# Kernel tuning notes

Hardware: AMD Instinct MI355X
Metric: run time of the kernel (lower is better)

Reference implementation:

```python
import jax, jax.numpy as jnp
import numpy as np

N_NODES = 100000
N_EDGES = 1600000
NFEAT, NHID, NOUT = 128, 64, 32


def setup_inputs() -> dict:
    key = jax.random.key(0)
    ks = jax.random.split(key, 8)
    x = jax.random.normal(ks[0], (N_NODES, NFEAT), dtype=jnp.float32)
    adj_vals = jax.random.uniform(ks[1], (N_EDGES,), dtype=jnp.float32)
    W1 = jax.random.normal(ks[2], (NFEAT, NHID), dtype=jnp.float32) * (1.0 / np.sqrt(NFEAT))
    b1 = jnp.zeros((NHID,), dtype=jnp.float32)
    W2 = jax.random.normal(ks[3], (NHID, NOUT), dtype=jnp.float32) * (1.0 / np.sqrt(NHID))
    b2 = jnp.zeros((NOUT,), dtype=jnp.float32)
    edge_src = jax.random.randint(ks[4], (N_EDGES,), 0, N_NODES, dtype=jnp.int32)
    edge_dst = jax.random.randint(ks[5], (N_EDGES,), 0, N_NODES, dtype=jnp.int32)
    return {"x": x, "adj_vals": adj_vals, "W1": W1, "b1": b1, "W2": W2,
            "b2": b2, "edge_src": edge_src, "edge_dst": edge_dst}


def spmm(vals, src, dst, dense, n_nodes):
    # out[i, :] = sum_{e : dst[e]==i} vals[e] * dense[src[e], :]
    gathered = dense[src] * vals[:, None]          # [E, D] gather (memory-bound)
    return jax.ops.segment_sum(gathered, dst, num_segments=n_nodes)


def reference(x, adj_vals, W1, b1, W2, b2, edge_src, edge_dst):
    # GraphConvolution 1: support = x @ W1; out = adj @ support + b1; relu
    h = spmm(adj_vals, edge_src, edge_dst, x @ W1, N_NODES) + b1
    h = jax.nn.relu(h)
    # dropout is identity in eval mode (training=False)
    # GraphConvolution 2
    out = spmm(adj_vals, edge_src, edge_dst, h @ W2, N_NODES) + b2
    return out
```

## Files before the change

### kernel.cpp

```cpp
#include <hip/hip_runtime.h>
#include <hip/hip_fp16.h>

#define N_NODES 100000
#define N_EDGES 1600000
#define NFEAT 128
#define NHID 64
#define NOUT 32

#define NPB 256
#define NB ((N_NODES + NPB - 1) / NPB)
#define CAP 4608
#define CCH 4096
#define NCH ((N_EDGES + CCH - 1) / CCH)
#define G1B ((N_NODES / 16 + 7) / 8)

typedef _Float16 half8 __attribute__((ext_vector_type(8)));
typedef float floatx4 __attribute__((ext_vector_type(4)));

__device__ __forceinline__ int wave_incl_scan(int v, int lane) {
#pragma unroll
    for (int d = 1; d < 64; d <<= 1) {
        int t = __shfl_up(v, d, 64);
        if (lane >= d) v += t;
    }
    return v;
}
__device__ __forceinline__ int block_excl_scan_512(int tsum, int tid, int* w8) {
    const int lane = tid & 63, wid = tid >> 6;
    int incl = wave_incl_scan(tsum, lane);
    if (lane == 63) w8[wid] = incl;
    __syncthreads();
    int wbase = 0;
#pragma unroll
    for (int i = 0; i < 7; ++i)
        if (wid > i) wbase += w8[i];
    return wbase + incl - tsum;
}

__global__ __launch_bounds__(64) void prep_kernel(const float* __restrict__ W1,
                                                  const float* __restrict__ W2,
                                                  __half* __restrict__ wfrag,
                                                  __half* __restrict__ w2frag,
                                                  int* __restrict__ gcur) {
    const int l = threadIdx.x;
    const int b = blockIdx.x;
    if (b < 16) {
        const int ks = b >> 2, ct = b & 3;
        const int kb = ks * 32 + (l >> 4) * 8;
        const int c  = ct * 16 + (l & 15);
        union { __half2 h2[4]; uint4 u; } pk;
#pragma unroll
        for (int j = 0; j < 4; ++j)
            pk.h2[j] = __floats2half2_rn(W1[(kb + 2 * j) * NHID + c],
                                         W1[(kb + 2 * j + 1) * NHID + c]);
        *(uint4*)&wfrag[((size_t)b * 64 + l) * 8] = pk.u;
    } else if (b < 20) {
        const int bb = b - 16;
        const int ks = bb >> 1, ct = bb & 1;
        const int kb = ks * 32 + (l >> 4) * 8;
        const int c  = ct * 16 + (l & 15);
        union { __half2 h2[4]; uint4 u; } pk;
#pragma unroll
        for (int j = 0; j < 4; ++j)
            pk.h2[j] = __floats2half2_rn(W2[(kb + 2 * j) * NOUT + c],
                                         W2[(kb + 2 * j + 1) * NOUT + c]);
        *(uint4*)&w2frag[((size_t)bb * 64 + l) * 8] = pk.u;
    } else {
        int i = (b - 20) * 64 + l;
        if (i < NB) gcur[i] = i * CAP;
    }
}

__global__ __launch_bounds__(512) void g1cs_kernel(const float* __restrict__ x,
                                                   const __half* __restrict__ wfrag,
                                                   __half* __restrict__ support,
                                                   const float* __restrict__ vals,
                                                   const int* __restrict__ src,
                                                   const int* __restrict__ dst,
                                                   int* __restrict__ gcur,
                                                   uint2* __restrict__ recsC) {
    __shared__ int cnt[NB];
    __shared__ int pos[NB];
    const int tid = threadIdx.x;

    if (blockIdx.x < NCH) {
        const int cbase0 = blockIdx.x * CCH;
        for (int i = tid; i < NB; i += 512) cnt[i] = 0;
        int dstv[CCH / 512];
        __syncthreads();
#pragma unroll
        for (int k = 0; k < CCH / 512; ++k) {
            int e = cbase0 + k * 512 + tid;
            int d = (e < N_EDGES) ? dst[e] : -1;
            dstv[k] = d;
            if (d >= 0) atomicAdd(&cnt[d >> 8], 1);
        }
        __syncthreads();
        for (int b = tid; b < NB; b += 512) {
            int c = cnt[b];
            pos[b] = c ? atomicAdd(&gcur[b], c) : 0;
        }
        __syncthreads();
#pragma unroll
        for (int k = 0; k < CCH / 512; ++k) {
            int e = cbase0 + k * 512 + tid;
            int d = dstv[k];
            if (d >= 0) {
                int b = d >> 8;
                int slot = atomicAdd(&pos[b], 1);
                if (slot < (b + 1) * CAP)
                    recsC[slot] = make_uint2((unsigned)src[e] |
                                             ((unsigned)(d & (NPB - 1)) << 17),
                                             __float_as_uint(vals[e]));
            }
        }
    } else {
        const int lane = tid & 63;
        const int tile = (blockIdx.x - NCH) * 8 + (tid >> 6);
        const int n0 = tile * 16;
        if (n0 >= N_NODES) return;

        half8 a[4][4];
#pragma unroll
        for (int ks = 0; ks < 4; ++ks)
#pragma unroll
            for (int ct = 0; ct < 4; ++ct)
                a[ks][ct] = *(const half8*)&wfrag[((size_t)(ks * 4 + ct) * 64 + lane) * 8];

        floatx4 acc[4];
#pragma unroll
        for (int ct = 0; ct < 4; ++ct) acc[ct] = (floatx4){0.f, 0.f, 0.f, 0.f};

        const int node = n0 + (lane & 15);
        const float* xrow = x + (size_t)node * NFEAT + (lane >> 4) * 8;

#pragma unroll
        for (int ks = 0; ks < 4; ++ks) {
            float4 f0 = *(const float4*)(xrow + ks * 32);
            float4 f1 = *(const float4*)(xrow + ks * 32 + 4);
            union { __half2 h2[4]; half8 v; } bv;
            bv.h2[0] = __floats2half2_rn(f0.x, f0.y);
            bv.h2[1] = __floats2half2_rn(f0.z, f0.w);
            bv.h2[2] = __floats2half2_rn(f1.x, f1.y);
            bv.h2[3] = __floats2half2_rn(f1.z, f1.w);
#pragma unroll
            for (int ct = 0; ct < 4; ++ct)
                acc[ct] = __builtin_amdgcn_mfma_f32_16x16x32_f16(a[ks][ct], bv.v, acc[ct], 0, 0, 0);
        }

        __half* srow = support + (size_t)node * NHID + (lane >> 4) * 4;
#pragma unroll
        for (int ct = 0; ct < 4; ++ct) {
            union { __half2 h2[2]; uint2 u; } pk;
            pk.h2[0] = __floats2half2_rn(acc[ct][0], acc[ct][1]);
            pk.h2[1] = __floats2half2_rn(acc[ct][2], acc[ct][3]);
            *(uint2*)&srow[ct * 16] = pk.u;
        }
    }
}

__global__ __launch_bounds__(512) void fine_sort_kernel(const int* __restrict__ gcur,
                                                        const uint2* __restrict__ recsC,
                                                        uint2* __restrict__ recs2,
                                                        int* __restrict__ offs,
                                                        int* __restrict__ ends) {
    __shared__ int cnt[NPB];
    __shared__ int cur[NPB];
    __shared__ int w8[8];
    const int tid = threadIdx.x;
    const int b = blockIdx.x;
    const int s = b * CAP;
    const int e = min(gcur[b], s + CAP);
    if (tid < NPB) cnt[tid] = 0;
    __syncthreads();
    for (int i = s + tid; i < e; i += 512)
        atomicAdd(&cnt[(recsC[i].x >> 17) & (NPB - 1)], 1);
    __syncthreads();
    int v = (tid < NPB) ? cnt[tid] : 0;
    int excl = block_excl_scan_512(v, tid, w8);
    if (tid < NPB) {
        cur[tid] = excl;
        const int node = b * NPB + tid;
        if (node < N_NODES) {
            offs[node] = s + excl;
            ends[node] = s + excl + v;
        }
    }
    __syncthreads();
    for (int i = s + tid; i < e; i += 512) {
        uint2 r = recsC[i];
        int dl = (r.x >> 17) & (NPB - 1);
        int p = atomicAdd(&cur[dl], 1);
        recs2[s + p] = make_uint2(r.x & 0x1FFFF, r.y);
    }
}

__global__ __launch_bounds__(256) void spmm1_kernel(const int* __restrict__ offs,
                                                    const int* __restrict__ ends,
                                                    const uint2* __restrict__ recs,
                                                    const __half* __restrict__ dense,
                                                    const float* __restrict__ b1,
                                                    __half* __restrict__ h) {
    __shared__ float red[4][8][65];
    const int tid = threadIdx.x;
    const int lane = tid & 63;
    const int wid = tid >> 6;
    const int d = blockIdx.x * 4 + wid;
    if (d >= N_NODES) return;
    const int g = lane >> 3, q = lane & 7;
    __half2 hacc[4];
#pragma unroll
    for (int j = 0; j < 4; ++j) hacc[j] = __half2half2(__float2half(0.f));

    const int start = offs[d], end = ends[d];
    for (int e = start + g; e < end; e += 8) {
        uint2 r = recs[e];
        __half2 hv2 = __half2half2(__float2half(__uint_as_float(r.y)));
        union { uint4 u; __half2 h2[4]; } rw;
        rw.u = *(const uint4*)((const char*)dense + ((size_t)r.x << 7) + (q << 4));
#pragma unroll
        for (int j = 0; j < 4; ++j)
            hacc[j] = __hfma2(rw.h2[j], hv2, hacc[j]);
    }
#pragma unroll
    for (int j = 0; j < 4; ++j) {
        float2 f = __half22float2(hacc[j]);
        red[wid][g][q * 8 + 2 * j]     = f.x;
        red[wid][g][q * 8 + 2 * j + 1] = f.y;
    }
    __builtin_amdgcn_wave_barrier();
    float s = 0.f;
#pragma unroll
    for (int gg = 0; gg < 8; ++gg) s += red[wid][gg][lane];
    float hv = fmaxf(s + b1[lane], 0.f);
    h[(size_t)d * NHID + lane] = __float2half(hv);
}

__global__ __launch_bounds__(256) void gemm2_kernel(const __half* __restrict__ h,
                                                    const __half* __restrict__ w2frag,
                                                    __half* __restrict__ s2) {
    const int lane = threadIdx.x & 63;
    const int tile = blockIdx.x * 4 + (threadIdx.x >> 6);
    const int n0 = tile * 16;
    if (n0 >= N_NODES) return;

    half8 a[2][2];
#pragma unroll
    for (int ks = 0; ks < 2; ++ks)
#pragma unroll
        for (int ct = 0; ct < 2; ++ct)
            a[ks][ct] = *(const half8*)&w2frag[((size_t)(ks * 2 + ct) * 64 + lane) * 8];

    floatx4 acc[2];
#pragma unroll
    for (int ct = 0; ct < 2; ++ct) acc[ct] = (floatx4){0.f, 0.f, 0.f, 0.f};

    const int node = n0 + (lane & 15);
    const __half* hrow = h + (size_t)node * NHID + (lane >> 4) * 8;

#pragma unroll
    for (int ks = 0; ks < 2; ++ks) {
        half8 bv = *(const half8*)(hrow + ks * 32);
#pragma unroll
        for (int ct = 0; ct < 2; ++ct)
            acc[ct] = __builtin_amdgcn_mfma_f32_16x16x32_f16(a[ks][ct], bv, acc[ct], 0, 0, 0);
    }

    __half* srow = s2 + (size_t)node * NOUT + (lane >> 4) * 4;
#pragma unroll
    for (int ct = 0; ct < 2; ++ct) {
        union { __half2 h2[2]; uint2 u; } pk;
        pk.h2[0] = __floats2half2_rn(acc[ct][0], acc[ct][1]);
        pk.h2[1] = __floats2half2_rn(acc[ct][2], acc[ct][3]);
        *(uint2*)&srow[ct * 16] = pk.u;
    }
}

__global__ __launch_bounds__(256) void spmm2_kernel(const int* __restrict__ offs,
                                                    const int* __restrict__ ends,
                                                    const uint2* __restrict__ recs,
                                                    const __half* __restrict__ dense,
                                                    const float* __restrict__ b2,
                                                    float* __restrict__ out) {
    __shared__ float red[4][16][33];
    const int tid = threadIdx.x;
    const int lane = tid & 63;
    const int wid = tid >> 6;
    const int d = blockIdx.x * 4 + wid;
    if (d >= N_NODES) return;
    const int g = lane >> 2, q = lane & 3;
    __half2 hacc[4];
#pragma unroll
    for (int j = 0; j < 4; ++j) hacc[j] = __half2half2(__float2half(0.f));

    const int start = offs[d], end = ends[d];
    for (int e = start + g; e < end; e += 16) {
        uint2 r = recs[e];
        __half2 hv2 = __half2half2(__float2half(__uint_as_float(r.y)));
        union { uint4 u; __half2 h2[4]; } rw;
        rw.u = *(const uint4*)((const char*)dense + ((size_t)r.x << 6) + (q << 4));
#pragma unroll
        for (int j = 0; j < 4; ++j)
            hacc[j] = __hfma2(rw.h2[j], hv2, hacc[j]);
    }
#pragma unroll
    for (int j = 0; j < 4; ++j) {
        float2 f = __half22float2(hacc[j]);
        red[wid][g][q * 8 + 2 * j]     = f.x;
        red[wid][g][q * 8 + 2 * j + 1] = f.y;
    }
    __builtin_amdgcn_wave_barrier();
    const int f = lane & 31, hi = lane >> 5;
    float s = 0.f;
#pragma unroll
    for (int t = 0; t < 8; ++t) s += red[wid][hi * 8 + t][f];
    s += __shfl_xor(s, 32, 64);
    if (hi == 0) out[(size_t)d * NOUT + f] = s + b2[f];
}

extern "C" void kernel_launch(void* const* d_in, const int* in_sizes, int n_in,
                              void* d_out, int out_size, void* d_ws, size_t ws_size,
                              hipStream_t stream) {
    const float* x        = (const float*)d_in[0];
    const float* adj_vals = (const float*)d_in[1];
    const float* W1       = (const float*)d_in[2];
    const float* b1       = (const float*)d_in[3];
    const float* W2       = (const float*)d_in[4];
    const float* b2       = (const float*)d_in[5];
    const int*   esrc     = (const int*)d_in[6];
    const int*   edst     = (const int*)d_in[7];
    float*       out      = (float*)d_out;

    char* W = (char*)d_ws;
    __half* support = (__half*)W;
    __half* h       = (__half*)(W + 12800000);
    uint2*  recsC   = (uint2*)(W + 25600000);
    uint2*  recs2   = (uint2*)(W + 25600000 + (size_t)NB * CAP * 8);
    int*    IW      = (int*)(W + 25600000 + 2 * (size_t)NB * CAP * 8);
    int*    offs    = IW;
    int*    ends    = IW + 100032;
    int*    gcur    = IW + 200064;
    __half* wfrag   = (__half*)(IW + 200064 + 512);
    __half* w2frag  = wfrag + 8192;
    __half* s2      = support;

    prep_kernel<<<20 + (NB + 63) / 64, 64, 0, stream>>>(W1, W2, wfrag, w2frag, gcur);

    g1cs_kernel<<<NCH + G1B, 512, 0, stream>>>(x, wfrag, support,
                                               adj_vals, esrc, edst, gcur, recsC);

    fine_sort_kernel<<<NB, 512, 0, stream>>>(gcur, recsC, recs2, offs, ends);

    spmm1_kernel<<<(N_NODES + 3) / 4, 256, 0, stream>>>(offs, ends, recs2,
                                                        support, b1, h);

    gemm2_kernel<<<(N_NODES / 16 + 3) / 4, 256, 0, stream>>>(h, w2frag, s2);

    spmm2_kernel<<<(N_NODES + 3) / 4, 256, 0, stream>>>(offs, ends, recs2,
                                                        s2, b2, out);
}
```

Measured before the change: 134.3 us.

## Split SpMM kernels into feature-column slices with more edges per wave

Both SpMM kernels now split the feature dimension into 16-column slices handled by separate blocks (4 slices for layer 1, 2 for layer 2). Each wave walks 32 edges at once, with two lanes per edge each loading 16 bytes. Slices run in block order, so each pass gathers from a narrower column band of the dense matrix, which may improve cache locality and gives more edge-level parallelism per node. The cost is that the edge records and offsets are read once per slice, and each gathered row access brings in only 32 bytes instead of a full row.

Result: slower. 225.7 us (+68.0%).

```diff
diff --git a/kernel.cpp b/kernel.cpp
--- a/kernel.cpp
+++ b/kernel.cpp
@@ -13,6 +13,7 @@
 #define CCH 4096
 #define NCH ((N_EDGES + CCH - 1) / CCH)
 #define G1B ((N_NODES / 16 + 7) / 8)
+#define SQB (N_NODES / 4)
 
 typedef _Float16 half8 __attribute__((ext_vector_type(8)));
 typedef float floatx4 __attribute__((ext_vector_type(4)));
@@ -201,23 +202,25 @@
                                                     const __half* __restrict__ dense,
                                                     const float* __restrict__ b1,
                                                     __half* __restrict__ h) {
-    __shared__ float red[4][8][65];
+    __shared__ float red[4][32][17];
     const int tid = threadIdx.x;
     const int lane = tid & 63;
     const int wid = tid >> 6;
-    const int d = blockIdx.x * 4 + wid;
-    if (d >= N_NODES) return;
-    const int g = lane >> 3, q = lane & 7;
+    const int slice = blockIdx.x / SQB;
+    const int nq = blockIdx.x - slice * SQB;
+    const int d = nq * 4 + wid;
+    const int p = lane >> 1, sub = lane & 1;
     __half2 hacc[4];
 #pragma unroll
     for (int j = 0; j < 4; ++j) hacc[j] = __half2half2(__float2half(0.f));
 
     const int start = offs[d], end = ends[d];
-    for (int e = start + g; e < end; e += 8) {
+    const char* dbase = (const char*)dense + slice * 32 + sub * 16;
+    for (int e = start + p; e < end; e += 32) {
         uint2 r = recs[e];
         __half2 hv2 = __half2half2(__float2half(__uint_as_float(r.y)));
         union { uint4 u; __half2 h2[4]; } rw;
-        rw.u = *(const uint4*)((const char*)dense + ((size_t)r.x << 7) + (q << 4));
+        rw.u = *(const uint4*)(dbase + ((size_t)r.x << 7));
 #pragma unroll
         for (int j = 0; j < 4; ++j)
             hacc[j] = __hfma2(rw.h2[j], hv2, hacc[j]);
@@ -225,15 +228,21 @@
 #pragma unroll
     for (int j = 0; j < 4; ++j) {
         float2 f = __half22float2(hacc[j]);
-        red[wid][g][q * 8 + 2 * j]     = f.x;
-        red[wid][g][q * 8 + 2 * j + 1] = f.y;
+        red[wid][p][sub * 8 + 2 * j]     = f.x;
+        red[wid][p][sub * 8 + 2 * j + 1] = f.y;
     }
     __builtin_amdgcn_wave_barrier();
+    const int c = lane & 15, chunk = lane >> 4;
     float s = 0.f;
 #pragma unroll
-    for (int gg = 0; gg < 8; ++gg) s += red[wid][gg][lane];
-    float hv = fmaxf(s + b1[lane], 0.f);
-    h[(size_t)d * NHID + lane] = __float2half(hv);
+    for (int t = 0; t < 8; ++t) s += red[wid][chunk * 8 + t][c];
+    s += __shfl_xor(s, 16, 64);
+    s += __shfl_xor(s, 32, 64);
+    if (chunk == 0) {
+        const int col = slice * 16 + c;
+        float hv = fmaxf(s + b1[col], 0.f);
+        h[(size_t)d * NHID + col] = __float2half(hv);
+    }
 }
 
 __global__ __launch_bounds__(256) void gemm2_kernel(const __half* __restrict__ h,
@@ -282,23 +291,25 @@
                                                     const __half* __restrict__ dense,
                                                     const float* __restrict__ b2,
                                                     float* __restrict__ out) {
-    __shared__ float red[4][16][33];
+    __shared__ float red[4][32][17];
     const int tid = threadIdx.x;
     const int lane = tid & 63;
     const int wid = tid >> 6;
-    const int d = blockIdx.x * 4 + wid;
-    if (d >= N_NODES) return;
-    const int g = lane >> 2, q = lane & 3;
+    const int slice = blockIdx.x / SQB;
+    const int nq = blockIdx.x - slice * SQB;
+    const int d = nq * 4 + wid;
+    const int p = lane >> 1, sub = lane & 1;
     __half2 hacc[4];
 #pragma unroll
     for (int j = 0; j < 4; ++j) hacc[j] = __half2half2(__float2half(0.f));
 
     const int start = offs[d], end = ends[d];
-    for (int e = start + g; e < end; e += 16) {
+    const char* dbase = (const char*)dense + slice * 32 + sub * 16;
+    for (int e = start + p; e < end; e += 32) {
         uint2 r = recs[e];
         __half2 hv2 = __half2half2(__float2half(__uint_as_float(r.y)));
         union { uint4 u; __half2 h2[4]; } rw;
-        rw.u = *(const uint4*)((const char*)dense + ((size_t)r.x << 6) + (q << 4));
+        rw.u = *(const uint4*)(dbase + ((size_t)r.x << 6));
 #pragma unroll
         for (int j = 0; j < 4; ++j)
             hacc[j] = __hfma2(rw.h2[j], hv2, hacc[j]);
@@ -306,16 +317,20 @@
 #pragma unroll
     for (int j = 0; j < 4; ++j) {
         float2 f = __half22float2(hacc[j]);
-        red[wid][g][q * 8 + 2 * j]     = f.x;
-        red[wid][g][q * 8 + 2 * j + 1] = f.y;
+        red[wid][p][sub * 8 + 2 * j]     = f.x;
+        red[wid][p][sub * 8 + 2 * j + 1] = f.y;
     }
     __builtin_amdgcn_wave_barrier();
-    const int f = lane & 31, hi = lane >> 5;
+    const int c = lane & 15, chunk = lane >> 4;
     float s = 0.f;
 #pragma unroll
-    for (int t = 0; t < 8; ++t) s += red[wid][hi * 8 + t][f];
+    for (int t = 0; t < 8; ++t) s += red[wid][chunk * 8 + t][c];
+    s += __shfl_xor(s, 16, 64);
     s += __shfl_xor(s, 32, 64);
-    if (hi == 0) out[(size_t)d * NOUT + f] = s + b2[f];
+    if (chunk == 0) {
+        const int col = slice * 16 + c;
+        out[(size_t)d * NOUT + col] = s + b2[col];
+    }
 }
 
 extern "C" void kernel_launch(void* const* d_in, const int* in_sizes, int n_in,
@@ -351,11 +366,9 @@
 
     fine_sort_kernel<<<NB, 512, 0, stream>>>(gcur, recsC, recs2, offs, ends);
 
-    spmm1_kernel<<<(N_NODES + 3) / 4, 256, 0, stream>>>(offs, ends, recs2,
-                                                        support, b1, h);
+    spmm1_kernel<<<4 * SQB, 256, 0, stream>>>(offs, ends, recs2, support, b1, h);
 
     gemm2_kernel<<<(N_NODES / 16 + 3) / 4, 256, 0, stream>>>(h, w2frag, s2);
 
-    spmm2_kernel<<<(N_NODES + 3) / 4, 256, 0, stream>>>(offs, ends, recs2,
-                                                        s2, b2, out);
-}
+    spmm2_kernel<<<2 * SQB, 256, 0, stream>>>(offs, ends, recs2, s2, b2, out);
+}
```

## Split hidden features into column slices and pack edge records to 32 bits

Applied to the files above, without the earlier changes.

The support and hidden matrices are stored as two 32-column slices, each laid out contiguously per node, and spmm1 runs as two passes, one per slice, with 64-byte rows. Each pass's gathered working set is half as large, which should give better L2 hit rates for the random gathers. Edge records are packed into one 32-bit word holding a 17-bit source index and a 15-bit half value with the sign bit dropped, since the values are non-negative. This halves record traffic in both spmm kernels, at the cost of reading the edge list twice in spmm1.

Result: slower. 148.6 us (+10.6%).

```diff
diff --git a/kernel.cpp b/kernel.cpp
--- a/kernel.cpp
+++ b/kernel.cpp
@@ -13,6 +13,7 @@
 #define CCH 4096
 #define NCH ((N_EDGES + CCH - 1) / CCH)
 #define G1B ((N_NODES / 16 + 7) / 8)
+#define SQB (N_NODES / 4)
 
 typedef _Float16 half8 __attribute__((ext_vector_type(8)));
 typedef float floatx4 __attribute__((ext_vector_type(4)));
@@ -148,20 +149,21 @@
                 acc[ct] = __builtin_amdgcn_mfma_f32_16x16x32_f16(a[ks][ct], bv.v, acc[ct], 0, 0, 0);
         }
 
-        __half* srow = support + (size_t)node * NHID + (lane >> 4) * 4;
 #pragma unroll
         for (int ct = 0; ct < 4; ++ct) {
+            __half* srow = support + (size_t)(ct >> 1) * N_NODES * 32 +
+                           (size_t)node * 32 + (ct & 1) * 16 + (lane >> 4) * 4;
             union { __half2 h2[2]; uint2 u; } pk;
             pk.h2[0] = __floats2half2_rn(acc[ct][0], acc[ct][1]);
             pk.h2[1] = __floats2half2_rn(acc[ct][2], acc[ct][3]);
-            *(uint2*)&srow[ct * 16] = pk.u;
+            *(uint2*)srow = pk.u;
         }
     }
 }
 
 __global__ __launch_bounds__(512) void fine_sort_kernel(const int* __restrict__ gcur,
                                                         const uint2* __restrict__ recsC,
-                                                        uint2* __restrict__ recs2,
+                                                        unsigned* __restrict__ recs2,
                                                         int* __restrict__ offs,
                                                         int* __restrict__ ends) {
     __shared__ int cnt[NPB];
@@ -190,34 +192,37 @@
     for (int i = s + tid; i < e; i += 512) {
         uint2 r = recsC[i];
         int dl = (r.x >> 17) & (NPB - 1);
+        unsigned hb = (unsigned)__half_as_ushort(__float2half(__uint_as_float(r.y))) & 0x7FFFu;
         int p = atomicAdd(&cur[dl], 1);
-        recs2[s + p] = make_uint2(r.x & 0x1FFFF, r.y);
+        recs2[s + p] = (r.x & 0x1FFFFu) | (hb << 17);
     }
 }
 
 __global__ __launch_bounds__(256) void spmm1_kernel(const int* __restrict__ offs,
                                                     const int* __restrict__ ends,
-                                                    const uint2* __restrict__ recs,
-                                                    const __half* __restrict__ dense,
+                                                    const unsigned* __restrict__ recs,
+                                                    const __half* __restrict__ support,
                                                     const float* __restrict__ b1,
                                                     __half* __restrict__ h) {
-    __shared__ float red[4][8][65];
+    __shared__ float red[4][16][33];
     const int tid = threadIdx.x;
     const int lane = tid & 63;
     const int wid = tid >> 6;
-    const int d = blockIdx.x * 4 + wid;
-    if (d >= N_NODES) return;
-    const int g = lane >> 3, q = lane & 7;
+    const int slice = blockIdx.x / SQB;
+    const int nq = blockIdx.x - slice * SQB;
+    const int d = nq * 4 + wid;
+    const int g = lane >> 2, q4 = lane & 3;
     __half2 hacc[4];
 #pragma unroll
     for (int j = 0; j < 4; ++j) hacc[j] = __half2half2(__float2half(0.f));
 
     const int start = offs[d], end = ends[d];
-    for (int e = start + g; e < end; e += 8) {
-        uint2 r = recs[e];
-        __half2 hv2 = __half2half2(__float2half(__uint_as_float(r.y)));
+    const char* dbase = (const char*)(support + (size_t)slice * N_NODES * 32) + (q4 << 4);
+    for (int e = start + g; e < end; e += 16) {
+        unsigned r = recs[e];
+        __half2 hv2 = __half2half2(__ushort_as_half((unsigned short)(r >> 17)));
         union { uint4 u; __half2 h2[4]; } rw;
-        rw.u = *(const uint4*)((const char*)dense + ((size_t)r.x << 7) + (q << 4));
+        rw.u = *(const uint4*)(dbase + ((size_t)(r & 0x1FFFFu) << 6));
 #pragma unroll
         for (int j = 0; j < 4; ++j)
             hacc[j] = __hfma2(rw.h2[j], hv2, hacc[j]);
@@ -225,15 +230,19 @@
 #pragma unroll
     for (int j = 0; j < 4; ++j) {
         float2 f = __half22float2(hacc[j]);
-        red[wid][g][q * 8 + 2 * j]     = f.x;
-        red[wid][g][q * 8 + 2 * j + 1] = f.y;
+        red[wid][g][q4 * 8 + 2 * j]     = f.x;
+        red[wid][g][q4 * 8 + 2 * j + 1] = f.y;
     }
     __builtin_amdgcn_wave_barrier();
+    const int c = lane & 31, chunk = lane >> 5;
     float s = 0.f;
 #pragma unroll
-    for (int gg = 0; gg < 8; ++gg) s += red[wid][gg][lane];
-    float hv = fmaxf(s + b1[lane], 0.f);
-    h[(size_t)d * NHID + lane] = __float2half(hv);
+    for (int t = 0; t < 8; ++t) s += red[wid][chunk * 8 + t][c];
+    s += __shfl_xor(s, 32, 64);
+    if (chunk == 0) {
+        float hv = fmaxf(s + b1[slice * 32 + c], 0.f);
+        h[(size_t)slice * N_NODES * 32 + (size_t)d * 32 + c] = __float2half(hv);
+    }
 }
 
 __global__ __launch_bounds__(256) void gemm2_kernel(const __half* __restrict__ h,
@@ -256,11 +265,11 @@
     for (int ct = 0; ct < 2; ++ct) acc[ct] = (floatx4){0.f, 0.f, 0.f, 0.f};
 
     const int node = n0 + (lane & 15);
-    const __half* hrow = h + (size_t)node * NHID + (lane >> 4) * 8;
+    const __half* h0 = h + (size_t)node * 32 + (lane >> 4) * 8;
 
 #pragma unroll
     for (int ks = 0; ks < 2; ++ks) {
-        half8 bv = *(const half8*)(hrow + ks * 32);
+        half8 bv = *(const half8*)(h0 + (size_t)ks * N_NODES * 32);
 #pragma unroll
         for (int ct = 0; ct < 2; ++ct)
             acc[ct] = __builtin_amdgcn_mfma_f32_16x16x32_f16(a[ks][ct], bv, acc[ct], 0, 0, 0);
@@ -278,7 +287,7 @@
 
 __global__ __launch_bounds__(256) void spmm2_kernel(const int* __restrict__ offs,
                                                     const int* __restrict__ ends,
-                                                    const uint2* __restrict__ recs,
+                                                    const unsigned* __restrict__ recs,
                                                     const __half* __restrict__ dense,
                                                     const float* __restrict__ b2,
                                                     float* __restrict__ out) {
@@ -288,17 +297,18 @@
     const int wid = tid >> 6;
     const int d = blockIdx.x * 4 + wid;
     if (d >= N_NODES) return;
-    const int g = lane >> 2, q = lane & 3;
+    const int g = lane >> 2, q4 = lane & 3;
     __half2 hacc[4];
 #pragma unroll
     for (int j = 0; j < 4; ++j) hacc[j] = __half2half2(__float2half(0.f));
 
     const int start = offs[d], end = ends[d];
+    const char* dbase = (const char*)dense + (q4 << 4);
     for (int e = start + g; e < end; e += 16) {
-        uint2 r = recs[e];
-        __half2 hv2 = __half2half2(__float2half(__uint_as_float(r.y)));
+        unsigned r = recs[e];
+        __half2 hv2 = __half2half2(__ushort_as_half((unsigned short)(r >> 17)));
         union { uint4 u; __half2 h2[4]; } rw;
-        rw.u = *(const uint4*)((const char*)dense + ((size_t)r.x << 6) + (q << 4));
+        rw.u = *(const uint4*)(dbase + ((size_t)(r & 0x1FFFFu) << 6));
 #pragma unroll
         for (int j = 0; j < 4; ++j)
             hacc[j] = __hfma2(rw.h2[j], hv2, hacc[j]);
@@ -306,16 +316,16 @@
 #pragma unroll
     for (int j = 0; j < 4; ++j) {
         float2 f = __half22float2(hacc[j]);
-        red[wid][g][q * 8 + 2 * j]     = f.x;
-        red[wid][g][q * 8 + 2 * j + 1] = f.y;
+        red[wid][g][q4 * 8 + 2 * j]     = f.x;
+        red[wid][g][q4 * 8 + 2 * j + 1] = f.y;
     }
     __builtin_amdgcn_wave_barrier();
-    const int f = lane & 31, hi = lane >> 5;
+    const int c = lane & 31, chunk = lane >> 5;
     float s = 0.f;
 #pragma unroll
-    for (int t = 0; t < 8; ++t) s += red[wid][hi * 8 + t][f];
+    for (int t = 0; t < 8; ++t) s += red[wid][chunk * 8 + t][c];
     s += __shfl_xor(s, 32, 64);
-    if (hi == 0) out[(size_t)d * NOUT + f] = s + b2[f];
+    if (chunk == 0) out[(size_t)d * NOUT + c] = s + b2[c];
 }
 
 extern "C" void kernel_launch(void* const* d_in, const int* in_sizes, int n_in,
@@ -332,17 +342,17 @@
     float*       out      = (float*)d_out;
 
     char* W = (char*)d_ws;
-    __half* support = (__half*)W;
-    __half* h       = (__half*)(W + 12800000);
-    uint2*  recsC   = (uint2*)(W + 25600000);
-    uint2*  recs2   = (uint2*)(W + 25600000 + (size_t)NB * CAP * 8);
-    int*    IW      = (int*)(W + 25600000 + 2 * (size_t)NB * CAP * 8);
-    int*    offs    = IW;
-    int*    ends    = IW + 100032;
-    int*    gcur    = IW + 200064;
-    __half* wfrag   = (__half*)(IW + 200064 + 512);
-    __half* w2frag  = wfrag + 8192;
-    __half* s2      = support;
+    __half*   support = (__half*)W;
+    __half*   h       = (__half*)(W + 12800000);
+    uint2*    recsC   = (uint2*)(W + 25600000);
+    unsigned* recs2   = (unsigned*)(W + 25600000 + (size_t)NB * CAP * 8);
+    int*      IW      = (int*)(W + 25600000 + (size_t)NB * CAP * 12);
+    int*      offs    = IW;
+    int*      ends    = IW + 100032;
+    int*      gcur    = IW + 200064;
+    __half*   wfrag   = (__half*)(IW + 200064 + 512);
+    __half*   w2frag  = wfrag + 8192;
+    __half*   s2      = support;
 
     prep_kernel<<<20 + (NB + 63) / 64, 64, 0, stream>>>(W1, W2, wfrag, w2frag, gcur);
 
@@ -351,8 +361,7 @@
 
     fine_sort_kernel<<<NB, 512, 0, stream>>>(gcur, recsC, recs2, offs, ends);
 
-    spmm1_kernel<<<(N_NODES + 3) / 4, 256, 0, stream>>>(offs, ends, recs2,
-                                                        support, b1, h);
+    spmm1_kernel<<<2 * SQB, 256, 0, stream>>>(offs, ends, recs2, support, b1, h);
 
     gemm2_kernel<<<(N_NODES / 16 + 3) / 4, 256, 0, stream>>>(h, w2frag, s2);
 
```
